# Kernel optimization log

Measured on AMD Instinct MI355X. Metric: run time of the kernel, lower is better.

The kernel has to match this reference:

```python
import jax, jax.numpy as jnp
import numpy as np
import math

HEAD_SIZE = 128
N_EMBED = 2048
B, T = 4, 4096
TOP_K_RATIO = 0.1


def setup_inputs() -> dict:
    key = jax.random.key(0)
    k1, k2, k3, k4 = jax.random.split(key, 4)
    index = jax.random.normal(k1, (B, T, N_EMBED), dtype=jnp.float32)
    s = 1.0 / math.sqrt(N_EMBED)
    Wq = jax.random.normal(k2, (N_EMBED, HEAD_SIZE), dtype=jnp.float32) * s
    Wk = jax.random.normal(k3, (N_EMBED, HEAD_SIZE), dtype=jnp.float32) * s
    Wv = jax.random.normal(k4, (N_EMBED, HEAD_SIZE), dtype=jnp.float32) * s
    return {"index": index, "Wq": Wq, "Wk": Wk, "Wv": Wv}


def reference(index, Wq, Wk, Wv):
    # memory = index (self-attention case)
    Bv, Tv, _ = index.shape
    top_k = int(TOP_K_RATIO * Tv)  # 409

    q = index @ Wq  # [B, T, D]
    k = index @ Wk
    v = index @ Wv

    q_norms = jnp.linalg.norm(q, axis=-1)  # [B, T]
    _, top_idx = jax.lax.top_k(q_norms, top_k)  # [B, K]

    idx = top_idx[..., None]  # [B, K, 1]
    q_topk = jnp.take_along_axis(q, idx, axis=1)  # [B, K, D]
    k_topk = jnp.take_along_axis(k, idx, axis=1)
    v_topk = jnp.take_along_axis(v, idx, axis=1)

    w = jnp.einsum('bid,bjd->bij', q_topk, k_topk) / math.sqrt(HEAD_SIZE)
    # eval mode: no causal mask (only applied in training), dropout = identity
    w = jax.nn.softmax(w, axis=-1)  # stable softmax (internal max subtraction)
    out_topk = w @ v_topk  # [B, K, D]

    batch_idx = jnp.arange(Bv)[:, None]  # [B, 1]
    output = jnp.zeros((Bv, Tv, HEAD_SIZE), dtype=out_topk.dtype)
    output = output.at[batch_idx, top_idx].add(out_topk)  # scatter_add (indices unique)
    return output
```

## Files before the change

kernel.cpp:

```cpp
#include <hip/hip_runtime.h>
#include <hip/hip_bf16.h>

#define NB 4
#define NT 4096
#define NC 2048
#define ND 128
#define NK 409
#define KPAD 416
#define NM (NB * NK)

typedef __attribute__((ext_vector_type(8))) short short8;
typedef __attribute__((ext_vector_type(4))) float f32x4;

union S8U { short8 v; ushort u[8]; };

__device__ __forceinline__ void split2(float x, ushort& h, ushort& l) {
    union { float f; unsigned u; } a; a.f = x;
    unsigned r = a.u + 0x7FFFu + ((a.u >> 16) & 1u);
    h = (ushort)(r >> 16);
    union { unsigned u; float f; } hb; hb.u = ((unsigned)h) << 16;
    float res = x - hb.f;
    union { float f; unsigned u; } b; b.f = res;
    unsigned r2 = b.u + 0x7FFFu + ((b.u >> 16) & 1u);
    l = (ushort)(r2 >> 16);
}

__device__ __forceinline__ uint4 pack8(const ushort* s) {
    uint4 v;
    v.x = (unsigned)s[0] | ((unsigned)s[1] << 16);
    v.y = (unsigned)s[2] | ((unsigned)s[3] << 16);
    v.z = (unsigned)s[4] | ((unsigned)s[5] << 16);
    v.w = (unsigned)s[6] | ((unsigned)s[7] << 16);
    return v;
}

__device__ __forceinline__ int slotOf(int n, int lq) {
    return n * 4 + ((lq + (n >> 1)) & 3);
}

__global__ __launch_bounds__(256) void bconv_tiles(
    const float* __restrict__ W, ushort* __restrict__ Bt)
{
    const int kt = blockIdx.x;
    const int t = threadIdx.x;
    const int n = t & 127;
    const int lq0 = (t >> 7) * 2;
    #pragma unroll
    for (int e = 0; e < 2; ++e) {
        int lq = lq0 + e;
        ushort h[8], l[8];
        #pragma unroll
        for (int j = 0; j < 8; ++j) {
            float x = W[(size_t)(kt * 32 + lq * 8 + j) * ND + n];
            split2(x, h[j], l[j]);
        }
        int slot = slotOf(n, lq);
        *(uint4*)&Bt[((size_t)(kt * 2 + 0) * 512 + slot) * 8] = pack8(h);
        *(uint4*)&Bt[((size_t)(kt * 2 + 1) * 512 + slot) * 8] = pack8(l);
    }
}

#define QSPLIT 2
__global__ __launch_bounds__(256) void qgemm_v5(
    const float* __restrict__ A, const ushort* __restrict__ Bt,
    float* __restrict__ q1, float* __restrict__ q2)
{
    const int tid = threadIdx.x;
    const int w = tid >> 6, lane = tid & 63;
    const int lrow = lane & 15, lq = lane >> 4;
    const int m0 = blockIdx.x * 64;
    const int KITER = (NC / QSPLIT) / 32;
    const int kt0 = blockIdx.y * KITER;
    const int kb = blockIdx.y * (NC / QSPLIT);

    const float* arow = A + (size_t)(m0 + w * 16 + lrow) * NC + kb + lq * 8;

    int boff[8];
    #pragma unroll
    for (int ni = 0; ni < 8; ++ni)
        boff[ni] = slotOf(ni * 16 + lrow, lq) * 8;

    f32x4 acc[8];
    #pragma unroll
    for (int i = 0; i < 8; ++i) acc[i] = (f32x4){0.f, 0.f, 0.f, 0.f};

    short8 bhA[8], blA[8], bhB[8], blB[8];
    {
        const ushort* gb = Bt + (size_t)kt0 * 8192;
        #pragma unroll
        for (int ni = 0; ni < 8; ++ni) {
            bhA[ni] = *(const short8*)(gb + boff[ni]);
            blA[ni] = *(const short8*)(gb + 4096 + boff[ni]);
        }
    }
    float4 fa0 = *(const float4*)(arow + 0);
    float4 fa1 = *(const float4*)(arow + 4);

#define QSTEP(BHC, BLC, BHN, BLN, KT)                                         \
    {                                                                         \
        short8 ah, al;                                                        \
        {                                                                     \
            S8U H, L;                                                         \
            float xs[8] = {fa0.x, fa0.y, fa0.z, fa0.w,                        \
                           fa1.x, fa1.y, fa1.z, fa1.w};                       \
            _Pragma("unroll")                                                 \
            for (int j = 0; j < 8; ++j) split2(xs[j], H.u[j], L.u[j]);        \
            ah = H.v; al = L.v;                                               \
        }                                                                     \
        const int ktn = ((KT) + 1 < KITER) ? (KT) + 1 : (KT);                 \
        const ushort* gbn = Bt + (size_t)(kt0 + ktn) * 8192;                  \
        _Pragma("unroll")                                                     \
        for (int ni = 0; ni < 8; ++ni) {                                      \
            BHN[ni] = *(const short8*)(gbn + boff[ni]);                       \
            BLN[ni] = *(const short8*)(gbn + 4096 + boff[ni]);                \
        }                                                                     \
        fa0 = *(const float4*)(arow + ktn * 32);                              \
        fa1 = *(const float4*)(arow + ktn * 32 + 4);                          \
        _Pragma("unroll")                                                     \
        for (int ni = 0; ni < 8; ++ni) {                                      \
            acc[ni] = __builtin_amdgcn_mfma_f32_16x16x32_bf16(ah, BHC[ni], acc[ni], 0, 0, 0); \
            acc[ni] = __builtin_amdgcn_mfma_f32_16x16x32_bf16(ah, BLC[ni], acc[ni], 0, 0, 0); \
            acc[ni] = __builtin_amdgcn_mfma_f32_16x16x32_bf16(al, BHC[ni], acc[ni], 0, 0, 0); \
        }                                                                     \
    }

    for (int kt = 0; kt < KITER; kt += 2) {
        QSTEP(bhA, blA, bhB, blB, kt);
        QSTEP(bhB, blB, bhA, blA, kt + 1);
    }
#undef QSTEP

    float* __restrict__ qd = blockIdx.y ? q2 : q1;
    #pragma unroll
    for (int ni = 0; ni < 8; ++ni) {
        const int col = ni * 16 + lrow;
        #pragma unroll
        for (int r = 0; r < 4; ++r) {
            const int grow = m0 + w * 16 + lq * 4 + r;
            qd[(size_t)grow * ND + col] = acc[ni][r];
        }
    }
}

#define KVSPLIT 8
__global__ __launch_bounds__(256) void kvgemm_v5(
    const float* __restrict__ X, const ushort* __restrict__ Bkt,
    const ushort* __restrict__ Bvt, const int* __restrict__ topi,
    float* __restrict__ ktop, float* __restrict__ vtop)
{
    const int tid = threadIdx.x;
    const int w = tid >> 6, lane = tid & 63;
    const int lrow = lane & 15, lq = lane >> 4;
    const int m0 = blockIdx.x * 64;
    const int KITER = (NC / KVSPLIT) / 32;
    const int kt0 = blockIdx.y * KITER;
    const int kb = blockIdx.y * (NC / KVSPLIT);
    const ushort* __restrict__ Bt = blockIdx.z ? Bvt : Bkt;

    const int gi = m0 + w * 16 + lrow;
    const int giC = gi < NM ? gi : NM - 1;
    const int b = giC / NK, ii = giC % NK;
    const int src = topi[b * KPAD + ii];
    const float* arow = X + ((size_t)b * NT + src) * NC + kb + lq * 8;

    int boff[8];
    #pragma unroll
    for (int ni = 0; ni < 8; ++ni)
        boff[ni] = slotOf(ni * 16 + lrow, lq) * 8;

    f32x4 acc[8];
    #pragma unroll
    for (int i = 0; i < 8; ++i) acc[i] = (f32x4){0.f, 0.f, 0.f, 0.f};

    short8 bhA[8], blA[8], bhB[8], blB[8];
    {
        const ushort* gb = Bt + (size_t)kt0 * 8192;
        #pragma unroll
        for (int ni = 0; ni < 8; ++ni) {
            bhA[ni] = *(const short8*)(gb + boff[ni]);
            blA[ni] = *(const short8*)(gb + 4096 + boff[ni]);
        }
    }
    float4 fa0 = *(const float4*)(arow + 0);
    float4 fa1 = *(const float4*)(arow + 4);

#define QSTEP(BHC, BLC, BHN, BLN, KT)                                         \
    {                                                                         \
        short8 ah, al;                                                        \
        {                                                                     \
            S8U H, L;                                                         \
            float xs[8] = {fa0.x, fa0.y, fa0.z, fa0.w,                        \
                           fa1.x, fa1.y, fa1.z, fa1.w};                       \
            _Pragma("unroll")                                                 \
            for (int j = 0; j < 8; ++j) split2(xs[j], H.u[j], L.u[j]);        \
            ah = H.v; al = L.v;                                               \
        }                                                                     \
        const int ktn = ((KT) + 1 < KITER) ? (KT) + 1 : (KT);                 \
        const ushort* gbn = Bt + (size_t)(kt0 + ktn) * 8192;                  \
        _Pragma("unroll")                                                     \
        for (int ni = 0; ni < 8; ++ni) {                                      \
            BHN[ni] = *(const short8*)(gbn + boff[ni]);                       \
            BLN[ni] = *(const short8*)(gbn + 4096 + boff[ni]);                \
        }                                                                     \
        fa0 = *(const float4*)(arow + ktn * 32);                              \
        fa1 = *(const float4*)(arow + ktn * 32 + 4);                          \
        _Pragma("unroll")                                                     \
        for (int ni = 0; ni < 8; ++ni) {                                      \
            acc[ni] = __builtin_amdgcn_mfma_f32_16x16x32_bf16(ah, BHC[ni], acc[ni], 0, 0, 0); \
            acc[ni] = __builtin_amdgcn_mfma_f32_16x16x32_bf16(ah, BLC[ni], acc[ni], 0, 0, 0); \
            acc[ni] = __builtin_amdgcn_mfma_f32_16x16x32_bf16(al, BHC[ni], acc[ni], 0, 0, 0); \
        }                                                                     \
    }

    for (int kt = 0; kt < KITER; kt += 2) {
        QSTEP(bhA, blA, bhB, blB, kt);
        QSTEP(bhB, blB, bhA, blA, kt + 1);
    }
#undef QSTEP

    float* __restrict__ dst = blockIdx.z ? vtop : ktop;
    #pragma unroll
    for (int ni = 0; ni < 8; ++ni) {
        const int col = ni * 16 + lrow;
        #pragma unroll
        for (int r = 0; r < 4; ++r) {
            const int grow = m0 + w * 16 + lq * 4 + r;
            if (grow < NM)
                atomicAdd(&dst[(size_t)grow * ND + col], acc[ni][r]);
        }
    }
}

__global__ __launch_bounds__(256) void qnorm_kernel(
    float* __restrict__ q1, const float* __restrict__ q2, float* __restrict__ qn)
{
    const int wv = (blockIdx.x * 256 + threadIdx.x) >> 6;
    const int lane = threadIdx.x & 63;
    float* r1 = q1 + (size_t)wv * ND;
    const float* r2 = q2 + (size_t)wv * ND;
    float a = r1[lane] + r2[lane];
    float b = r1[lane + 64] + r2[lane + 64];
    r1[lane] = a;
    r1[lane + 64] = b;
    float s = a * a + b * b;
    #pragma unroll
    for (int off = 32; off > 0; off >>= 1) s += __shfl_xor(s, off);
    if (lane == 0) qn[wv] = sqrtf(s);
}

__global__ __launch_bounds__(256) void topk_kernel(
    const float* __restrict__ qn, int* __restrict__ topi, int* __restrict__ cnt)
{
    __shared__ int rs[4][64];
    const int b = blockIdx.y;
    const int is = threadIdx.x & 63;
    const int i = blockIdx.x * 64 + is;
    const int chunk = threadIdx.x >> 6;
    const float vi = qn[(size_t)b * NT + i];
    const float4* qv = (const float4*)(qn + (size_t)b * NT + chunk * 1024);
    int rank = 0;
    #pragma unroll 4
    for (int j4 = 0; j4 < 256; ++j4) {
        float4 v = qv[j4];
        int j = chunk * 1024 + j4 * 4;
        rank += (v.x > vi || (v.x == vi && (j + 0) < i)) ? 1 : 0;
        rank += (v.y > vi || (v.y == vi && (j + 1) < i)) ? 1 : 0;
        rank += (v.z > vi || (v.z == vi && (j + 2) < i)) ? 1 : 0;
        rank += (v.w > vi || (v.w == vi && (j + 3) < i)) ? 1 : 0;
    }
    rs[chunk][is] = rank;
    __syncthreads();
    if (threadIdx.x < 64) {
        int rk = rs[0][threadIdx.x] + rs[1][threadIdx.x] + rs[2][threadIdx.x] + rs[3][threadIdx.x];
        if (rk < NK) {
            int p = atomicAdd(&cnt[b], 1);
            topi[b * KPAD + p] = blockIdx.x * 64 + threadIdx.x;
        }
    }
}

__global__ __launch_bounds__(256) void attn_kernel(
    const float* __restrict__ q, const float* __restrict__ ktop,
    const float* __restrict__ vtop, const int* __restrict__ topi,
    float* __restrict__ out)
{
    __shared__ float qs[ND];
    __shared__ float ss[KPAD];
    __shared__ float red[256];
    __shared__ float pv[2][ND];
    const int bi = blockIdx.x;
    const int b = bi / NK, i = bi % NK;
    const int t = threadIdx.x;
    const int row = topi[b * KPAD + i];
    if (t < ND) qs[t] = q[((size_t)b * NT + row) * ND + t];
    __syncthreads();

    const float scale = 0.08838834764831844f;
    float mymax = -1e30f;
    #pragma unroll
    for (int rep = 0; rep < 2; ++rep) {
        int j = t + rep * 256;
        if (j < NK) {
            const float4* kr = (const float4*)(ktop + ((size_t)b * NK + j) * ND);
            const float4* q4 = (const float4*)qs;
            float s = 0.f;
            #pragma unroll
            for (int dd = 0; dd < 32; ++dd) {
                float4 a = q4[dd], kv = kr[dd];
                s += a.x * kv.x + a.y * kv.y + a.z * kv.z + a.w * kv.w;
            }
            s *= scale;
            ss[j] = s;
            mymax = fmaxf(mymax, s);
        }
    }
    red[t] = mymax;
    __syncthreads();
    for (int off = 128; off > 0; off >>= 1) {
        if (t < off) red[t] = fmaxf(red[t], red[t + off]);
        __syncthreads();
    }
    const float mx = red[0];
    __syncthreads();

    float mysum = 0.f;
    #pragma unroll
    for (int rep = 0; rep < 2; ++rep) {
        int j = t + rep * 256;
        if (j < NK) {
            float p = __expf(ss[j] - mx);
            ss[j] = p;
            mysum += p;
        }
    }
    red[t] = mysum;
    __syncthreads();
    for (int off = 128; off > 0; off >>= 1) {
        if (t < off) red[t] += red[t + off];
        __syncthreads();
    }
    const float inv = 1.f / red[0];

    const int col = t & (ND - 1), half = t >> 7;
    float o = 0.f;
    #pragma unroll 4
    for (int j = half; j < NK; j += 2)
        o = fmaf(ss[j], vtop[((size_t)b * NK + j) * ND + col], o);
    pv[half][col] = o;
    __syncthreads();
    if (t < ND)
        out[((size_t)b * NT + row) * ND + t] = (pv[0][t] + pv[1][t]) * inv;
}

extern "C" void kernel_launch(void* const* d_in, const int* in_sizes, int n_in,
                              void* d_out, int out_size, void* d_ws, size_t ws_size,
                              hipStream_t stream)
{
    const float* index = (const float*)d_in[0];
    const float* Wq = (const float*)d_in[1];
    const float* Wk = (const float*)d_in[2];
    const float* Wv = (const float*)d_in[3];
    float* out = (float*)d_out;

    char* ws = (char*)d_ws;
    float*  q1   = (float*)(ws);
    float*  qn   = (float*)(ws + 8388608);
    int*    topi = (int*)  (ws + 8454144);
    int*    cnt  = (int*)  (ws + 8462336);
    ushort* Bqt  = (ushort*)(ws + 8462592);
    float*  ktop = (float*)(ws + 8462592);
    float*  vtop = (float*)(ws + 9300224);

    float*  q2  = (float*)d_out;
    ushort* Bkt = (ushort*)d_out;
    ushort* Bvt = (ushort*)((char*)d_out + 1048576);

    hipMemsetAsync(cnt, 0, NB * sizeof(int), stream);

    bconv_tiles<<<dim3(64), dim3(256), 0, stream>>>(Wq, Bqt);
    qgemm_v5<<<dim3(NB * NT / 64, QSPLIT), dim3(256), 0, stream>>>(index, Bqt, q1, q2);
    qnorm_kernel<<<dim3(NB * NT / 4), dim3(256), 0, stream>>>(q1, q2, qn);
    topk_kernel<<<dim3(NT / 64, NB), dim3(256), 0, stream>>>(qn, topi, cnt);
    bconv_tiles<<<dim3(64), dim3(256), 0, stream>>>(Wk, Bkt);
    bconv_tiles<<<dim3(64), dim3(256), 0, stream>>>(Wv, Bvt);
    hipMemsetAsync(ktop, 0, 2 * 837632, stream);
    kvgemm_v5<<<dim3((NM + 63) / 64, KVSPLIT, 2), dim3(256), 0, stream>>>(
        index, Bkt, Bvt, topi, ktop, vtop);
    hipMemsetAsync(d_out, 0, (size_t)out_size * sizeof(float), stream);
    attn_kernel<<<dim3(NM), dim3(256), 0, stream>>>(q1, ktop, vtop, topi, out);
}
```

Baseline: 370.3 us.

## Split Q GEMM K-range across two wave groups with shared-memory reduction

The Q projection GEMM now runs 512-thread blocks in which two groups of four waves each take half of the block's K range (16 iterations instead of 32), and their accumulators are combined through an LDS buffer before storing. This halves the serial K loop per wave and raises the number of waves in flight, aiming to hide the global load latency of the register-streamed A and B operands. The price is a 32 KB shared-memory reduction, a block barrier, and higher register pressure under the new launch bounds. The QSTEP macro is also hoisted so both GEMM kernels share it.

```diff
diff --git a/kernel.cpp b/kernel.cpp
--- a/kernel.cpp
+++ b/kernel.cpp
@@ -59,42 +59,6 @@
         *(uint4*)&Bt[((size_t)(kt * 2 + 1) * 512 + slot) * 8] = pack8(l);
     }
 }
-
-#define QSPLIT 2
-__global__ __launch_bounds__(256) void qgemm_v5(
-    const float* __restrict__ A, const ushort* __restrict__ Bt,
-    float* __restrict__ q1, float* __restrict__ q2)
-{
-    const int tid = threadIdx.x;
-    const int w = tid >> 6, lane = tid & 63;
-    const int lrow = lane & 15, lq = lane >> 4;
-    const int m0 = blockIdx.x * 64;
-    const int KITER = (NC / QSPLIT) / 32;
-    const int kt0 = blockIdx.y * KITER;
-    const int kb = blockIdx.y * (NC / QSPLIT);
-
-    const float* arow = A + (size_t)(m0 + w * 16 + lrow) * NC + kb + lq * 8;
-
-    int boff[8];
-    #pragma unroll
-    for (int ni = 0; ni < 8; ++ni)
-        boff[ni] = slotOf(ni * 16 + lrow, lq) * 8;
-
-    f32x4 acc[8];
-    #pragma unroll
-    for (int i = 0; i < 8; ++i) acc[i] = (f32x4){0.f, 0.f, 0.f, 0.f};
-
-    short8 bhA[8], blA[8], bhB[8], blB[8];
-    {
-        const ushort* gb = Bt + (size_t)kt0 * 8192;
-        #pragma unroll
-        for (int ni = 0; ni < 8; ++ni) {
-            bhA[ni] = *(const short8*)(gb + boff[ni]);
-            blA[ni] = *(const short8*)(gb + 4096 + boff[ni]);
-        }
-    }
-    float4 fa0 = *(const float4*)(arow + 0);
-    float4 fa1 = *(const float4*)(arow + 4);
 
 #define QSTEP(BHC, BLC, BHN, BLN, KT)                                         \
     {                                                                         \
@@ -124,20 +88,75 @@
         }                                                                     \
     }
 
+#define QSPLIT 2
+__global__ __launch_bounds__(512, 4) void qgemm_v7(
+    const float* __restrict__ A, const ushort* __restrict__ Bt,
+    float* __restrict__ q1, float* __restrict__ q2)
+{
+    __shared__ __align__(16) float RED[4][64][32];
+
+    const int tid = threadIdx.x;
+    const int w = tid >> 6, lane = tid & 63;
+    const int rg = w & 3, kh = w >> 2;
+    const int lrow = lane & 15, lq = lane >> 4;
+    const int m0 = blockIdx.x * 64;
+    const int KITER = 16;
+    const int kt0 = (blockIdx.y * 2 + kh) * 16;
+    const int kb = blockIdx.y * 1024 + kh * 512;
+
+    const float* arow = A + (size_t)(m0 + rg * 16 + lrow) * NC + kb + lq * 8;
+
+    int boff[8];
+    #pragma unroll
+    for (int ni = 0; ni < 8; ++ni)
+        boff[ni] = slotOf(ni * 16 + lrow, lq) * 8;
+
+    f32x4 acc[8];
+    #pragma unroll
+    for (int i = 0; i < 8; ++i) acc[i] = (f32x4){0.f, 0.f, 0.f, 0.f};
+
+    short8 bhA[8], blA[8], bhB[8], blB[8];
+    {
+        const ushort* gb = Bt + (size_t)kt0 * 8192;
+        #pragma unroll
+        for (int ni = 0; ni < 8; ++ni) {
+            bhA[ni] = *(const short8*)(gb + boff[ni]);
+            blA[ni] = *(const short8*)(gb + 4096 + boff[ni]);
+        }
+    }
+    float4 fa0 = *(const float4*)(arow + 0);
+    float4 fa1 = *(const float4*)(arow + 4);
+
     for (int kt = 0; kt < KITER; kt += 2) {
         QSTEP(bhA, blA, bhB, blB, kt);
         QSTEP(bhB, blB, bhA, blA, kt + 1);
     }
-#undef QSTEP
-
-    float* __restrict__ qd = blockIdx.y ? q2 : q1;
-    #pragma unroll
-    for (int ni = 0; ni < 8; ++ni) {
-        const int col = ni * 16 + lrow;
-        #pragma unroll
-        for (int r = 0; r < 4; ++r) {
-            const int grow = m0 + w * 16 + lq * 4 + r;
-            qd[(size_t)grow * ND + col] = acc[ni][r];
+
+    if (kh == 1) {
+        #pragma unroll
+        for (int c = 0; c < 8; ++c) {
+            int ch = (c + lane) & 7;
+            *(f32x4*)&RED[rg][lane][ch * 4] = acc[ch];
+        }
+    }
+    __syncthreads();
+    if (kh == 0) {
+        #pragma unroll
+        for (int c = 0; c < 8; ++c) {
+            int ch = (c + lane) & 7;
+            f32x4 o = *(const f32x4*)&RED[rg][lane][ch * 4];
+            acc[ch][0] += o[0]; acc[ch][1] += o[1];
+            acc[ch][2] += o[2]; acc[ch][3] += o[3];
+        }
+        float* __restrict__ qd = blockIdx.y ? q2 : q1;
+        #pragma unroll
+        for (int ni = 0; ni < 8; ++ni) {
+            const int col = ni * 16 + lrow;
+            #pragma unroll
+            for (int r = 0; r < 4; ++r) {
+                const int grow = m0 + rg * 16 + lq * 4 + r;
+                qd[(size_t)grow * ND + col] = acc[ni][r];
+            }
         }
     }
 }
@@ -184,39 +203,10 @@
     float4 fa0 = *(const float4*)(arow + 0);
     float4 fa1 = *(const float4*)(arow + 4);
 
-#define QSTEP(BHC, BLC, BHN, BLN, KT)                                         \
-    {                                                                         \
-        short8 ah, al;                                                        \
-        {                                                                     \
-            S8U H, L;                                                         \
-            float xs[8] = {fa0.x, fa0.y, fa0.z, fa0.w,                        \
-                           fa1.x, fa1.y, fa1.z, fa1.w};                       \
-            _Pragma("unroll")                                                 \
-            for (int j = 0; j < 8; ++j) split2(xs[j], H.u[j], L.u[j]);        \
-            ah = H.v; al = L.v;                                               \
-        }                                                                     \
-        const int ktn = ((KT) + 1 < KITER) ? (KT) + 1 : (KT);                 \
-        const ushort* gbn = Bt + (size_t)(kt0 + ktn) * 8192;                  \
-        _Pragma("unroll")                                                     \
-        for (int ni = 0; ni < 8; ++ni) {                                      \
-            BHN[ni] = *(const short8*)(gbn + boff[ni]);                       \
-            BLN[ni] = *(const short8*)(gbn + 4096 + boff[ni]);                \
-        }                                                                     \
-        fa0 = *(const float4*)(arow + ktn * 32);                              \
-        fa1 = *(const float4*)(arow + ktn * 32 + 4);                          \
-        _Pragma("unroll")                                                     \
-        for (int ni = 0; ni < 8; ++ni) {                                      \
-            acc[ni] = __builtin_amdgcn_mfma_f32_16x16x32_bf16(ah, BHC[ni], acc[ni], 0, 0, 0); \
-            acc[ni] = __builtin_amdgcn_mfma_f32_16x16x32_bf16(ah, BLC[ni], acc[ni], 0, 0, 0); \
-            acc[ni] = __builtin_amdgcn_mfma_f32_16x16x32_bf16(al, BHC[ni], acc[ni], 0, 0, 0); \
-        }                                                                     \
-    }
-
     for (int kt = 0; kt < KITER; kt += 2) {
         QSTEP(bhA, blA, bhB, blB, kt);
         QSTEP(bhB, blB, bhA, blA, kt + 1);
     }
-#undef QSTEP
 
     float* __restrict__ dst = blockIdx.z ? vtop : ktop;
     #pragma unroll
@@ -378,7 +368,7 @@
     hipMemsetAsync(cnt, 0, NB * sizeof(int), stream);
 
     bconv_tiles<<<dim3(64), dim3(256), 0, stream>>>(Wq, Bqt);
-    qgemm_v5<<<dim3(NB * NT / 64, QSPLIT), dim3(256), 0, stream>>>(index, Bqt, q1, q2);
+    qgemm_v7<<<dim3(NB * NT / 64, QSPLIT), dim3(512), 0, stream>>>(index, Bqt, q1, q2);
     qnorm_kernel<<<dim3(NB * NT / 4), dim3(256), 0, stream>>>(q1, q2, qn);
     topk_kernel<<<dim3(NT / 64, NB), dim3(256), 0, stream>>>(qn, topi, cnt);
     bconv_tiles<<<dim3(64), dim3(256), 0, stream>>>(Wk, Bkt);
```

After: 396.1 us. 1.07x slower.
